# Kernel tuning notes

Hardware: AMD Instinct MI355X
Metric: run time of the kernel (lower is better)

The kernel has to match this reference:

```python
import jax, jax.numpy as jnp
import numpy as np

C = 256
D = C // 8  # query/key channels
B, H, W = 4, 64, 64


def setup_inputs() -> dict:
    key = jax.random.key(0)
    ks = jax.random.split(key, 9)
    s = 0.02
    return {
        "z": jax.random.normal(ks[0], (B, C, H, W), jnp.float32),
        "x": jax.random.normal(ks[1], (B, C, H, W), jnp.float32),
        "y": jax.random.normal(ks[2], (B, C, H, W), jnp.float32),
        "Wq": jax.random.normal(ks[3], (D, C), jnp.float32) * s,
        "bq": jnp.zeros((D,), jnp.float32),
        "Wk": jax.random.normal(ks[4], (D, C), jnp.float32) * s,
        "bk": jnp.zeros((D,), jnp.float32),
        "Wv": jax.random.normal(ks[5], (C, C), jnp.float32) * s,
        "bv": jnp.zeros((C,), jnp.float32),
    }


def reference(z, x, y, Wq, bq, Wk, bk, Wv, bv):
    b, c, h, w = x.shape
    n = h * w
    xf = x.reshape(b, c, n)  # [B,C,N]
    yf = y.reshape(b, c, n)
    zf = z.reshape(b, c, n)
    # 1x1 convs == channel-wise linear projections
    q = jnp.einsum("dc,bcn->bnd", Wq, xf) + bq                 # [B,N,D]
    k = jnp.einsum("dc,bcn->bdn", Wk, yf) + bk[:, None]        # [B,D,N]
    energy = jnp.einsum("bnd,bdm->bnm", q, k)                  # [B,N,N]
    attn = jax.nn.softmax(energy, axis=-1)                     # rows over keys
    v = jnp.einsum("ec,bcn->ben", Wv, zf) + bv[:, None]        # [B,C,N]
    # torch: bmm(value, attn^T) -> out[b,c,m] = sum_n v[b,c,n]*attn[b,m,n]
    out = jnp.einsum("ben,bmn->bem", v, attn)                  # [B,C,N]
    return z + out.reshape(b, c, h, w)
```

## Files before the change

kernel.cpp:

```cpp
#include <hip/hip_runtime.h>
#include <hip/hip_bf16.h>

#define Bn 4
#define Cn 256
#define Dn 32
#define Nn 4096

typedef __attribute__((ext_vector_type(8))) short short8;
typedef __attribute__((ext_vector_type(4))) float f32x4;

__device__ __forceinline__ unsigned short f2bf(float f) {
  union { __hip_bfloat16 h; unsigned short u; } c;
  c.h = __float2bfloat16(f);
  return c.u;
}

__global__ __launch_bounds__(640, 1) void SA_proj2(
    const float* __restrict__ x, const float* __restrict__ y, const float* __restrict__ z,
    const float* __restrict__ Wq, const float* __restrict__ bq,
    const float* __restrict__ Wk, const float* __restrict__ bk,
    const float* __restrict__ Wv, const float* __restrict__ bv,
    unsigned short* __restrict__ qws, unsigned short* __restrict__ kws,
    unsigned short* __restrict__ vws)
{
  __shared__ char lds[3 * 33280];
  const int bid = blockIdx.x, tid = threadIdx.x;
  const int lane = tid & 63, wv2 = tid >> 6;
  const int g = lane >> 4, l15 = lane & 15;
  const int b = bid >> 6, n0 = (bid & 63) << 6;

  const float* src0 = x + (size_t)b * Cn * Nn;
  const float* src1 = y + (size_t)b * Cn * Nn;
  const float* src2 = z + (size_t)b * Cn * Nn;

  const int isv = (wv2 >= 2);
  const float* W    = isv ? Wv : (wv2 == 0 ? Wq : Wk);
  const float* bias = isv ? bv : (wv2 == 0 ? bq : bk);
  const int e0w = isv ? ((wv2 - 2) << 5) : 0;
  const char* myT = lds + (isv ? 2 : wv2) * 33280;

  const int cl = tid >> 2, fq = tid & 3;

  f32x4 sl0[4], sl1[4], sl2[4];
  auto stage_ld = [&](int ck) {
    const size_t row = (size_t)(ck * 128 + cl) * Nn + n0 + fq * 4;
#pragma unroll
    for (int i = 0; i < 4; ++i) sl0[i] = *(const f32x4*)(src0 + row + i * 16);
#pragma unroll
    for (int i = 0; i < 4; ++i) sl1[i] = *(const f32x4*)(src1 + row + i * 16);
#pragma unroll
    for (int i = 0; i < 4; ++i) sl2[i] = *(const f32x4*)(src2 + row + i * 16);
  };
  auto stage_wr = [&](int ck) {
    const int cb = (ck * 128 + cl) * 2;
#pragma unroll
    for (int i = 0; i < 4; ++i)
#pragma unroll
      for (int j = 0; j < 4; ++j) {
        char* rp = lds + (size_t)(fq * 4 + i * 16 + j) * 520 + cb;
        *(unsigned short*)(rp)         = f2bf(sl0[i][j]);
        *(unsigned short*)(rp + 33280) = f2bf(sl1[i][j]);
        *(unsigned short*)(rp + 66560) = f2bf(sl2[i][j]);
      }
  };

  f32x4 wf[2][4][2];
  auto w_ld = [&](int ck) {
#pragma unroll
    for (int et = 0; et < 2; ++et) {
      const float* wp = W + (size_t)(e0w + 16 * et + l15) * 256 + ck * 128 + 4 * g;
#pragma unroll
      for (int cc = 0; cc < 4; ++cc) {
        wf[et][cc][0] = *(const f32x4*)(wp + cc * 32);
        wf[et][cc][1] = *(const f32x4*)(wp + cc * 32 + 16);
      }
    }
  };
  short8 af[2][4];
  auto w_cvt = [&]() {
#pragma unroll
    for (int et = 0; et < 2; ++et)
#pragma unroll
      for (int cc = 0; cc < 4; ++cc) {
        short8 t8;
#pragma unroll
        for (int j = 0; j < 4; ++j) {
          t8[j]     = (short)f2bf(wf[et][cc][0][j]);
          t8[4 + j] = (short)f2bf(wf[et][cc][1][j]);
        }
        af[et][cc] = t8;
      }
  };

  f32x4 acc[2][4];
#pragma unroll
  for (int et = 0; et < 2; ++et)
#pragma unroll
    for (int ns = 0; ns < 4; ++ns) { acc[et][ns][0]=0.f; acc[et][ns][1]=0.f; acc[et][ns][2]=0.f; acc[et][ns][3]=0.f; }

  auto compute = [&](int ck) {
#pragma unroll
    for (int cc = 0; cc < 4; ++cc) {
      const int cbyte = (ck * 128 + cc * 32 + 4 * g) * 2;
#pragma unroll
      for (int ns = 0; ns < 4; ++ns) {
        const char* rp = myT + (size_t)(16 * ns + l15) * 520 + cbyte;
        union { uint2 u[2]; short8 s; } bb;
        bb.u[0] = *(const uint2*)rp;
        bb.u[1] = *(const uint2*)(rp + 32);
#pragma unroll
        for (int et = 0; et < 2; ++et)
          acc[et][ns] = __builtin_amdgcn_mfma_f32_16x16x32_bf16(af[et][cc], bb.s, acc[et][ns], 0, 0, 0);
      }
    }
  };

  if (tid < 512) stage_ld(0);
  w_ld(0);
  if (tid < 512) stage_wr(0);
  __syncthreads();
  w_cvt();
  if (tid < 512) stage_ld(1);
  compute(0);
  if (tid < 512) stage_wr(1);
  w_ld(1);
  __syncthreads();
  w_cvt();
  compute(1);
  __syncthreads();

  float bvv[2][4];
#pragma unroll
  for (int et = 0; et < 2; ++et)
#pragma unroll
    for (int r = 0; r < 4; ++r) bvv[et][r] = bias[e0w + 16 * et + 4 * g + r];

  if (isv) {
#pragma unroll
    for (int et = 0; et < 2; ++et)
#pragma unroll
      for (int ns = 0; ns < 4; ++ns)
#pragma unroll
        for (int r = 0; r < 4; ++r) {
          int e = e0w + 16 * et + 4 * g + r;
          int n = 16 * ns + l15;
          *(unsigned short*)(lds + (size_t)e * 144 + n * 2) = f2bf(acc[et][ns][r] + bvv[et][r]);
        }
  } else {
    char* base = lds + (wv2 == 0 ? 66560 : 71680);
#pragma unroll
    for (int et = 0; et < 2; ++et)
#pragma unroll
      for (int ns = 0; ns < 4; ++ns)
#pragma unroll
        for (int r = 0; r < 4; ++r) {
          int d = 16 * et + 4 * g + r;
          int n = 16 * ns + l15;
          *(unsigned short*)(base + (size_t)n * 80 + d * 2) = f2bf(acc[et][ns][r] + bvv[et][r]);
        }
  }
  __syncthreads();

  if (tid < 512) {
    const int el = tid >> 1, half = tid & 1;
    char* gb = (char*)vws + (size_t)b * Cn * Nn * 2 + (size_t)el * Nn * 2 + (size_t)n0 * 2 + half * 64;
    const char* lb = lds + (size_t)el * 144 + half * 64;
#pragma unroll
    for (int i = 0; i < 4; ++i)
      *(uint4*)(gb + i * 16) = *(const uint4*)(lb + i * 16);
  }
  if (wv2 < 2) {
    unsigned short* ob = (wv2 == 0 ? qws : kws) + (size_t)b * Nn * Dn;
    const char* base = lds + (wv2 == 0 ? 66560 : 71680);
#pragma unroll
    for (int i = 0; i < 4; ++i) {
      int flat = 64 * i + lane;
      *(uint4*)((char*)ob + (size_t)n0 * 64 + flat * 16)
          = *(const uint4*)(base + (size_t)(flat >> 2) * 80 + (flat & 3) * 16);
    }
  }
}

__global__ __launch_bounds__(512, 2) void SA_flash(
    const unsigned short* __restrict__ qws, const unsigned short* __restrict__ kws,
    const unsigned short* __restrict__ vws, const float* __restrict__ z,
    float* __restrict__ outp)
{
  __shared__ char lds[83968];
  const int bid = blockIdx.x;
  const int b    = (bid >> 1) & 3;
  const int mblk = ((bid >> 3) << 1) | (bid & 1);
  const int m0 = mblk * 64;
  const int tid = threadIdx.x, lane = tid & 63;
  const int wv = tid >> 6, gg = wv >> 2, wq = wv & 3;
  const int g = lane >> 4, l15 = lane & 15;
  const int t2 = tid & 255;

  char* Kt = lds + gg * 41984;
  char* Vt = Kt + 5120;

  const unsigned short* qb = qws + (size_t)b * Nn * Dn;
  const unsigned short* kb = kws + (size_t)b * Nn * Dn;
  const unsigned short* vb = vws + (size_t)b * Cn * Nn;

  const int mw = m0 + 16 * wq;
  short8 qf;
  {
    const char* qp = (const char*)qb + (size_t)(mw + l15) * 64 + 8 * g;
    ushort4 q0 = *(const ushort4*)qp;
    ushort4 q1 = *(const ushort4*)(qp + 32);
    qf[0]=(short)q0.x; qf[1]=(short)q0.y; qf[2]=(short)q0.z; qf[3]=(short)q0.w;
    qf[4]=(short)q1.x; qf[5]=(short)q1.y; qf[6]=(short)q1.z; qf[7]=(short)q1.w;
  }

  f32x4 acc[16];
#pragma unroll
  for (int i = 0; i < 16; ++i) { acc[i][0]=0.f; acc[i][1]=0.f; acc[i][2]=0.f; acc[i][3]=0.f; }
  float m_run = -__builtin_inff(), l_run = 0.f;

  const int knl = t2 >> 2, kp = t2 & 3;
  uint4 kreg; uint4 vreg[8];
  auto stage_load = [&](int kt) {
    const int n0 = kt * 64;
    kreg = *(const uint4*)((const char*)kb + (size_t)(n0 + knl) * 64 + kp * 16);
#pragma unroll
    for (int i = 0; i < 8; ++i) {
      int idx = i * 256 + t2, e = idx >> 3, ch = idx & 7;
      vreg[i] = *(const uint4*)((const char*)vb + (size_t)e * (Nn * 2) + (size_t)(n0 + ch * 8) * 2);
    }
  };
  stage_load(gg);

  for (int it = 0; it < 32; ++it) {
    {
      int off1 = 32 * (kp & 1) + 8 * (kp >> 1);
      char* krow = Kt + (size_t)knl * 80;
      *(uint2*)(krow + off1)      = make_uint2(kreg.x, kreg.y);
      *(uint2*)(krow + off1 + 16) = make_uint2(kreg.z, kreg.w);
#pragma unroll
      for (int i = 0; i < 8; ++i) {
        int idx = i * 256 + t2, e = idx >> 3, ch = idx & 7;
        int p1 = 64 * (ch & 1) + 8 * (ch >> 1);
        char* vrow = Vt + (size_t)e * 144;
        *(uint2*)(vrow + p1)      = make_uint2(vreg[i].x, vreg[i].y);
        *(uint2*)(vrow + p1 + 32) = make_uint2(vreg[i].z, vreg[i].w);
      }
    }
    __syncthreads();
    if (it < 31) stage_load(2 * (it + 1) + gg);

    f32x4 s[4];
    const f32x4 zero4 = {0.f, 0.f, 0.f, 0.f};
#pragma unroll
    for (int t = 0; t < 4; ++t) {
      short8 kf = *(const short8*)(Kt + (size_t)(16*t + l15) * 80 + 16 * g);
      s[t] = __builtin_amdgcn_mfma_f32_16x16x32_bf16(kf, qf, zero4, 0, 0, 0);
    }
    float pm = s[0][0];
#pragma unroll
    for (int t = 0; t < 4; ++t)
#pragma unroll
      for (int r = 0; r < 4; ++r) pm = fmaxf(pm, s[t][r]);
    pm = fmaxf(pm, __shfl_xor(pm, 16, 64));
    pm = fmaxf(pm, __shfl_xor(pm, 32, 64));
    if (__any(pm > m_run)) {
      float mn = fmaxf(m_run, pm);
      float alpha = __expf(m_run - mn);
      l_run *= alpha;
      m_run = mn;
#pragma unroll
      for (int i = 0; i < 16; ++i) { acc[i][0]*=alpha; acc[i][1]*=alpha; acc[i][2]*=alpha; acc[i][3]*=alpha; }
    }
    float p[4][4]; float rs = 0.f;
#pragma unroll
    for (int t = 0; t < 4; ++t)
#pragma unroll
      for (int r = 0; r < 4; ++r) { float e = __expf(s[t][r] - m_run); p[t][r] = e; rs += e; }
    rs += __shfl_xor(rs, 16, 64);
    rs += __shfl_xor(rs, 32, 64);
    l_run += rs;

    short8 pf[2];
#pragma unroll
    for (int c = 0; c < 2; ++c) {
      short8 t8;
      t8[0]=(short)f2bf(p[2*c][0]);   t8[1]=(short)f2bf(p[2*c][1]);
      t8[2]=(short)f2bf(p[2*c][2]);   t8[3]=(short)f2bf(p[2*c][3]);
      t8[4]=(short)f2bf(p[2*c+1][0]); t8[5]=(short)f2bf(p[2*c+1][1]);
      t8[6]=(short)f2bf(p[2*c+1][2]); t8[7]=(short)f2bf(p[2*c+1][3]);
      pf[c] = t8;
    }
    __builtin_amdgcn_s_setprio(1);
#pragma unroll
    for (int c = 0; c < 2; ++c)
#pragma unroll
      for (int et = 0; et < 16; ++et) {
        short8 vf = *(const short8*)(Vt + (size_t)(16*et + l15) * 144 + 32 * g + 16 * c);
        acc[et] = __builtin_amdgcn_mfma_f32_16x16x32_bf16(vf, pf[c], acc[et], 0, 0, 0);
      }
    __builtin_amdgcn_s_setprio(0);
    __syncthreads();
  }

  __syncthreads();
  float* mz = (float*)(lds + 73728);
  mz[tid] = m_run;
  __syncthreads();
  float m_oth = mz[tid ^ 256];
  float M  = fmaxf(m_run, m_oth);
  float al = __expf(m_run - M);
  float l_sc = l_run * al;
  float* lz = (float*)(lds + 75776);
  if (gg == 1) {
    char* rowp = lds + (size_t)t2 * 272;
#pragma unroll
    for (int i = 0; i < 16; ++i) {
      f32x4 v = acc[i];
      v[0]*=al; v[1]*=al; v[2]*=al; v[3]*=al;
      *(f32x4*)(rowp + i*16) = v;
    }
    lz[t2] = l_sc;
  }
  __syncthreads();
  if (gg == 0) {
    char* rowp = lds + (size_t)t2 * 272;
    float inv = 1.0f / (l_sc + lz[t2]);
    const float* zb = z    + (size_t)b * Cn * Nn;
    float*       ob = outp + (size_t)b * Cn * Nn;
    const int mpos = mw + l15;
#pragma unroll
    for (int et = 0; et < 16; ++et) {
      f32x4 o = *(const f32x4*)(rowp + et*16);
#pragma unroll
      for (int r = 0; r < 4; ++r) {
        int e = 16*et + 4*g + r;
        size_t off = (size_t)e * Nn + mpos;
        ob[off] = zb[off] + (acc[et][r]*al + o[r]) * inv;
      }
    }
  }
}

extern "C" void kernel_launch(void* const* d_in, const int* in_sizes, int n_in,
                              void* d_out, int out_size, void* d_ws, size_t ws_size,
                              hipStream_t stream) {
  (void)in_sizes; (void)n_in; (void)out_size; (void)ws_size;
  const float* z  = (const float*)d_in[0];
  const float* x  = (const float*)d_in[1];
  const float* y  = (const float*)d_in[2];
  const float* Wq = (const float*)d_in[3];
  const float* bq = (const float*)d_in[4];
  const float* Wk = (const float*)d_in[5];
  const float* bk = (const float*)d_in[6];
  const float* Wv = (const float*)d_in[7];
  const float* bv = (const float*)d_in[8];
  float* out = (float*)d_out;

  unsigned short* qws = (unsigned short*)d_ws;
  unsigned short* kws = qws + (size_t)Bn * Nn * Dn;
  unsigned short* vws = kws + (size_t)Bn * Nn * Dn;

  SA_proj2<<<256, 640, 0, stream>>>(x, y, z, Wq, bq, Wk, bk, Wv, bv, qws, kws, vws);
  SA_flash<<<256, 512, 0, stream>>>(qws, kws, vws, z, out);
}
```

Baseline: 197.1 us.

## Pre-swizzle K/V into MFMA fragment layout and load directly to registers

The projection kernel now writes K and V to the workspace already arranged in the per-lane MFMA fragment order. The flash kernel can then load K and V straight from global memory into registers, skipping the LDS staging copy. The PV product is reorganized so each wave owns 64 output channels across all 64 queries. P fragments and per-row rescale factors are shared through LDS, with one barrier per iteration. This removes the LDS write/read traffic for K/V and shrinks LDS use, but adds a P exchange through LDS and a block-wide sync before rescaling.

```diff
diff --git a/kernel.cpp b/kernel.cpp
--- a/kernel.cpp
+++ b/kernel.cpp
@@ -8,6 +8,8 @@
 
 typedef __attribute__((ext_vector_type(8))) short short8;
 typedef __attribute__((ext_vector_type(4))) float f32x4;
+
+union U16 { uint4 u; short8 s; };
 
 __device__ __forceinline__ unsigned short f2bf(float f) {
   union { __hip_bfloat16 h; unsigned short u; } c;
@@ -28,6 +30,7 @@
   const int lane = tid & 63, wv2 = tid >> 6;
   const int g = lane >> 4, l15 = lane & 15;
   const int b = bid >> 6, n0 = (bid & 63) << 6;
+  const int kt = n0 >> 6;
 
   const float* src0 = x + (size_t)b * Cn * Nn;
   const float* src1 = y + (size_t)b * Cn * Nn;
@@ -105,9 +108,9 @@
 #pragma unroll
       for (int ns = 0; ns < 4; ++ns) {
         const char* rp = myT + (size_t)(16 * ns + l15) * 520 + cbyte;
-        union { uint2 u[2]; short8 s; } bb;
-        bb.u[0] = *(const uint2*)rp;
-        bb.u[1] = *(const uint2*)(rp + 32);
+        U16 bb;
+        bb.u.x = *(const unsigned*)rp;        bb.u.y = *(const unsigned*)(rp + 4);
+        bb.u.z = *(const unsigned*)(rp + 32); bb.u.w = *(const unsigned*)(rp + 36);
 #pragma unroll
         for (int et = 0; et < 2; ++et)
           acc[et][ns] = __builtin_amdgcn_mfma_f32_16x16x32_bf16(af[et][cc], bb.s, acc[et][ns], 0, 0, 0);
@@ -136,18 +139,19 @@
     for (int r = 0; r < 4; ++r) bvv[et][r] = bias[e0w + 16 * et + 4 * g + r];
 
   if (isv) {
+    const int vw = wv2 - 2, Wt = vw >> 1, w1 = vw & 1;
 #pragma unroll
     for (int et = 0; et < 2; ++et)
 #pragma unroll
       for (int ns = 0; ns < 4; ++ns)
 #pragma unroll
         for (int r = 0; r < 4; ++r) {
-          int e = e0w + 16 * et + 4 * g + r;
-          int n = 16 * ns + l15;
-          *(unsigned short*)(lds + (size_t)e * 144 + n * 2) = f2bf(acc[et][ns][r] + bvv[et][r]);
-        }
-  } else {
-    char* base = lds + (wv2 == 0 ? 66560 : 71680);
+          int byte = Wt * 8192 + (((2 * w1 + et) << 1) + (ns >> 1)) * 1024
+                   + ((l15 >> 2) * 16 + 4 * g + r) * 16 + (ns & 1) * 8 + (l15 & 3) * 2;
+          *(unsigned short*)(lds + byte) = f2bf(acc[et][ns][r] + bvv[et][r]);
+        }
+  } else if (wv2 == 0) {
+    char* base = lds + 66560;
 #pragma unroll
     for (int et = 0; et < 2; ++et)
 #pragma unroll
@@ -158,25 +162,41 @@
           int n = 16 * ns + l15;
           *(unsigned short*)(base + (size_t)n * 80 + d * 2) = f2bf(acc[et][ns][r] + bvv[et][r]);
         }
+  } else {
+    char* base = lds + 71680;
+#pragma unroll
+    for (int et = 0; et < 2; ++et)
+#pragma unroll
+      for (int ns = 0; ns < 4; ++ns)
+#pragma unroll
+        for (int r = 0; r < 4; ++r) {
+          int pos = ns * 1024 + g * 256 + l15 * 16 + et * 8 + r * 2;
+          *(unsigned short*)(base + pos) = f2bf(acc[et][ns][r] + bvv[et][r]);
+        }
   }
   __syncthreads();
 
   if (tid < 512) {
-    const int el = tid >> 1, half = tid & 1;
-    char* gb = (char*)vws + (size_t)b * Cn * Nn * 2 + (size_t)el * Nn * 2 + (size_t)n0 * 2 + half * 64;
-    const char* lb = lds + (size_t)el * 144 + half * 64;
+    char* gb = (char*)vws + (size_t)b * Cn * Nn * 2 + (size_t)kt * 32768 + tid * 64;
+    const char* lb = lds + tid * 64;
 #pragma unroll
     for (int i = 0; i < 4; ++i)
       *(uint4*)(gb + i * 16) = *(const uint4*)(lb + i * 16);
   }
-  if (wv2 < 2) {
-    unsigned short* ob = (wv2 == 0 ? qws : kws) + (size_t)b * Nn * Dn;
-    const char* base = lds + (wv2 == 0 ? 66560 : 71680);
+  if (wv2 == 0) {
+    unsigned short* ob = qws + (size_t)b * Nn * Dn;
 #pragma unroll
     for (int i = 0; i < 4; ++i) {
       int flat = 64 * i + lane;
       *(uint4*)((char*)ob + (size_t)n0 * 64 + flat * 16)
-          = *(const uint4*)(base + (size_t)(flat >> 2) * 80 + (flat & 3) * 16);
+          = *(const uint4*)(lds + 66560 + (size_t)(flat >> 2) * 80 + (flat & 3) * 16);
+    }
+  } else if (wv2 == 1) {
+    char* ob = (char*)kws + (size_t)b * Nn * Dn * 2 + (size_t)kt * 4096;
+#pragma unroll
+    for (int i = 0; i < 4; ++i) {
+      int flat = 64 * i + lane;
+      *(uint4*)(ob + flat * 16) = *(const uint4*)(lds + 71680 + flat * 16);
     }
   }
 }
@@ -186,7 +206,12 @@
     const unsigned short* __restrict__ vws, const float* __restrict__ z,
     float* __restrict__ outp)
 {
-  __shared__ char lds[83968];
+  __shared__ char lds[68608];
+  float*    m_arr = (float*)(lds + 66560);
+  float*    l_arr = (float*)(lds + 67072);
+  float*    a_arr = (float*)(lds + 67584);
+  unsigned* f_arr = (unsigned*)(lds + 68096);
+
   const int bid = blockIdx.x;
   const int b    = (bid >> 1) & 3;
   const int mblk = ((bid >> 3) << 1) | (bid & 1);
@@ -194,14 +219,12 @@
   const int tid = threadIdx.x, lane = tid & 63;
   const int wv = tid >> 6, gg = wv >> 2, wq = wv & 3;
   const int g = lane >> 4, l15 = lane & 15;
-  const int t2 = tid & 255;
-
-  char* Kt = lds + gg * 41984;
-  char* Vt = Kt + 5120;
+
+  char* Pg = lds + gg * 8192;
 
   const unsigned short* qb = qws + (size_t)b * Nn * Dn;
-  const unsigned short* kb = kws + (size_t)b * Nn * Dn;
-  const unsigned short* vb = vws + (size_t)b * Cn * Nn;
+  const char* kb = (const char*)kws + (size_t)b * Nn * Dn * 2;
+  const char* vb = (const char*)vws + (size_t)b * Cn * Nn * 2;
 
   const int mw = m0 + 16 * wq;
   short8 qf;
@@ -213,49 +236,36 @@
     qf[4]=(short)q1.x; qf[5]=(short)q1.y; qf[6]=(short)q1.z; qf[7]=(short)q1.w;
   }
 
-  f32x4 acc[16];
-#pragma unroll
-  for (int i = 0; i < 16; ++i) { acc[i][0]=0.f; acc[i][1]=0.f; acc[i][2]=0.f; acc[i][3]=0.f; }
+  f32x4 acc[4][4];
+#pragma unroll
+  for (int et = 0; et < 4; ++et)
+#pragma unroll
+    for (int qt = 0; qt < 4; ++qt) { acc[et][qt][0]=0.f; acc[et][qt][1]=0.f; acc[et][qt][2]=0.f; acc[et][qt][3]=0.f; }
   float m_run = -__builtin_inff(), l_run = 0.f;
 
-  const int knl = t2 >> 2, kp = t2 & 3;
-  uint4 kreg; uint4 vreg[8];
-  auto stage_load = [&](int kt) {
-    const int n0 = kt * 64;
-    kreg = *(const uint4*)((const char*)kb + (size_t)(n0 + knl) * 64 + kp * 16);
-#pragma unroll
-    for (int i = 0; i < 8; ++i) {
-      int idx = i * 256 + t2, e = idx >> 3, ch = idx & 7;
-      vreg[i] = *(const uint4*)((const char*)vb + (size_t)e * (Nn * 2) + (size_t)(n0 + ch * 8) * 2);
-    }
-  };
-  stage_load(gg);
+  uint4 kfr[4], vfr[8];
+  auto k_ld = [&](int t4) {
+    const char* p = kb + (size_t)t4 * 4096 + lane * 16;
+#pragma unroll
+    for (int t = 0; t < 4; ++t) kfr[t] = *(const uint4*)(p + t * 1024);
+  };
+  auto v_ld = [&](int t4) {
+    const char* p = vb + (size_t)t4 * 32768 + wq * 8192 + lane * 16;
+#pragma unroll
+    for (int f = 0; f < 8; ++f) vfr[f] = *(const uint4*)(p + f * 1024);
+  };
+  k_ld(gg); v_ld(gg);
 
   for (int it = 0; it < 32; ++it) {
-    {
-      int off1 = 32 * (kp & 1) + 8 * (kp >> 1);
-      char* krow = Kt + (size_t)knl * 80;
-      *(uint2*)(krow + off1)      = make_uint2(kreg.x, kreg.y);
-      *(uint2*)(krow + off1 + 16) = make_uint2(kreg.z, kreg.w);
-#pragma unroll
-      for (int i = 0; i < 8; ++i) {
-        int idx = i * 256 + t2, e = idx >> 3, ch = idx & 7;
-        int p1 = 64 * (ch & 1) + 8 * (ch >> 1);
-        char* vrow = Vt + (size_t)e * 144;
-        *(uint2*)(vrow + p1)      = make_uint2(vreg[i].x, vreg[i].y);
-        *(uint2*)(vrow + p1 + 32) = make_uint2(vreg[i].z, vreg[i].w);
-      }
-    }
-    __syncthreads();
-    if (it < 31) stage_load(2 * (it + 1) + gg);
-
     f32x4 s[4];
     const f32x4 zero4 = {0.f, 0.f, 0.f, 0.f};
 #pragma unroll
     for (int t = 0; t < 4; ++t) {
-      short8 kf = *(const short8*)(Kt + (size_t)(16*t + l15) * 80 + 16 * g);
-      s[t] = __builtin_amdgcn_mfma_f32_16x16x32_bf16(kf, qf, zero4, 0, 0, 0);
-    }
+      U16 ku; ku.u = kfr[t];
+      s[t] = __builtin_amdgcn_mfma_f32_16x16x32_bf16(ku.s, qf, zero4, 0, 0, 0);
+    }
+    if (it < 31) k_ld(2 * (it + 1) + gg);
+
     float pm = s[0][0];
 #pragma unroll
     for (int t = 0; t < 4; ++t)
@@ -263,13 +273,13 @@
       for (int r = 0; r < 4; ++r) pm = fmaxf(pm, s[t][r]);
     pm = fmaxf(pm, __shfl_xor(pm, 16, 64));
     pm = fmaxf(pm, __shfl_xor(pm, 32, 64));
-    if (__any(pm > m_run)) {
+    int trig = __any(pm > m_run);
+    float alpha = 1.0f;
+    if (trig) {
       float mn = fmaxf(m_run, pm);
-      float alpha = __expf(m_run - mn);
+      alpha = __expf(m_run - mn);
       l_run *= alpha;
       m_run = mn;
-#pragma unroll
-      for (int i = 0; i < 16; ++i) { acc[i][0]*=alpha; acc[i][1]*=alpha; acc[i][2]*=alpha; acc[i][3]*=alpha; }
     }
     float p[4][4]; float rs = 0.f;
 #pragma unroll
@@ -290,54 +300,93 @@
       t8[6]=(short)f2bf(p[2*c+1][2]); t8[7]=(short)f2bf(p[2*c+1][3]);
       pf[c] = t8;
     }
+    *(short8*)(Pg + (wq * 2 + 0) * 1024 + lane * 16) = pf[0];
+    *(short8*)(Pg + (wq * 2 + 1) * 1024 + lane * 16) = pf[1];
+    if (lane < 16) a_arr[gg * 64 + 16 * wq + lane] = alpha;
+    if (lane == 0) f_arr[gg * 4 + wq] = (unsigned)trig;
+    __syncthreads();
+
+    {
+      uint4 fl = *(const uint4*)(f_arr + gg * 4);
+      if (fl.x | fl.y | fl.z | fl.w) {
+        float al4[4];
+#pragma unroll
+        for (int qt = 0; qt < 4; ++qt) al4[qt] = a_arr[gg * 64 + 16 * qt + l15];
+#pragma unroll
+        for (int et = 0; et < 4; ++et)
+#pragma unroll
+          for (int qt = 0; qt < 4; ++qt) {
+            acc[et][qt][0]*=al4[qt]; acc[et][qt][1]*=al4[qt];
+            acc[et][qt][2]*=al4[qt]; acc[et][qt][3]*=al4[qt];
+          }
+      }
+    }
+
     __builtin_amdgcn_s_setprio(1);
 #pragma unroll
-    for (int c = 0; c < 2; ++c)
-#pragma unroll
-      for (int et = 0; et < 16; ++et) {
-        short8 vf = *(const short8*)(Vt + (size_t)(16*et + l15) * 144 + 32 * g + 16 * c);
-        acc[et] = __builtin_amdgcn_mfma_f32_16x16x32_bf16(vf, pf[c], acc[et], 0, 0, 0);
-      }
+    for (int qt = 0; qt < 4; ++qt) {
+#pragma unroll
+      for (int ks = 0; ks < 2; ++ks) {
+        short8 pfr = *(const short8*)(Pg + (qt * 2 + ks) * 1024 + lane * 16);
+#pragma unroll
+        for (int et = 0; et < 4; ++et) {
+          U16 vu; vu.u = vfr[et * 2 + ks];
+          acc[et][qt] = __builtin_amdgcn_mfma_f32_16x16x32_bf16(vu.s, pfr, acc[et][qt], 0, 0, 0);
+        }
+      }
+    }
     __builtin_amdgcn_s_setprio(0);
+    if (it < 31) v_ld(2 * (it + 1) + gg);
     __syncthreads();
   }
 
-  __syncthreads();
-  float* mz = (float*)(lds + 73728);
-  mz[tid] = m_run;
-  __syncthreads();
-  float m_oth = mz[tid ^ 256];
-  float M  = fmaxf(m_run, m_oth);
-  float al = __expf(m_run - M);
-  float l_sc = l_run * al;
-  float* lz = (float*)(lds + 75776);
+  if (lane < 16) {
+    m_arr[gg * 64 + 16 * wq + lane] = m_run;
+    l_arr[gg * 64 + 16 * wq + lane] = l_run;
+  }
+  __syncthreads();
+  float fmy[4], inv[4];
+#pragma unroll
+  for (int qt = 0; qt < 4; ++qt) {
+    int q = 16 * qt + l15;
+    float mv0 = m_arr[q], mv1 = m_arr[64 + q];
+    float lv0 = l_arr[q], lv1 = l_arr[64 + q];
+    float M = fmaxf(mv0, mv1);
+    float f0 = __expf(mv0 - M), f1 = __expf(mv1 - M);
+    inv[qt] = 1.0f / (lv0 * f0 + lv1 * f1);
+    fmy[qt] = gg ? f1 : f0;
+  }
+#pragma unroll
+  for (int et = 0; et < 4; ++et)
+#pragma unroll
+    for (int qt = 0; qt < 4; ++qt) {
+      acc[et][qt][0]*=fmy[qt]; acc[et][qt][1]*=fmy[qt];
+      acc[et][qt][2]*=fmy[qt]; acc[et][qt][3]*=fmy[qt];
+    }
   if (gg == 1) {
-    char* rowp = lds + (size_t)t2 * 272;
-#pragma unroll
-    for (int i = 0; i < 16; ++i) {
-      f32x4 v = acc[i];
-      v[0]*=al; v[1]*=al; v[2]*=al; v[3]*=al;
-      *(f32x4*)(rowp + i*16) = v;
-    }
-    lz[t2] = l_sc;
+#pragma unroll
+    for (int et = 0; et < 4; ++et)
+#pragma unroll
+      for (int qt = 0; qt < 4; ++qt)
+        *(f32x4*)(lds + (size_t)(16 * qt + l15) * 1040 + (64 * wq + 16 * et + 4 * g) * 4) = acc[et][qt];
   }
   __syncthreads();
   if (gg == 0) {
-    char* rowp = lds + (size_t)t2 * 272;
-    float inv = 1.0f / (l_sc + lz[t2]);
     const float* zb = z    + (size_t)b * Cn * Nn;
     float*       ob = outp + (size_t)b * Cn * Nn;
-    const int mpos = mw + l15;
-#pragma unroll
-    for (int et = 0; et < 16; ++et) {
-      f32x4 o = *(const f32x4*)(rowp + et*16);
-#pragma unroll
-      for (int r = 0; r < 4; ++r) {
-        int e = 16*et + 4*g + r;
-        size_t off = (size_t)e * Nn + mpos;
-        ob[off] = zb[off] + (acc[et][r]*al + o[r]) * inv;
-      }
-    }
+#pragma unroll
+    for (int et = 0; et < 4; ++et)
+#pragma unroll
+      for (int qt = 0; qt < 4; ++qt) {
+        f32x4 o = *(const f32x4*)(lds + (size_t)(16 * qt + l15) * 1040 + (64 * wq + 16 * et + 4 * g) * 4);
+        int q = m0 + 16 * qt + l15;
+#pragma unroll
+        for (int r = 0; r < 4; ++r) {
+          int e = 64 * wq + 16 * et + 4 * g + r;
+          size_t off = (size_t)e * Nn + q;
+          ob[off] = zb[off] + (acc[et][qt][r] + o[r]) * inv[qt];
+        }
+      }
   }
 }
 
```

Result: faster. 172.4 us (-12.5%).
